# Performance work log

Hardware: AMD Instinct MI355X
Metric: run time of the kernel (lower is better)

Reference implementation:

```python
import jax, jax.numpy as jnp
import numpy as np
import math

B, S, D, H, WIDTH, NHW = 8, 1024, 512, 8, 8, 2
DK = D // H
S2 = S + 2 * WIDTH


def setup_inputs() -> dict:
    key = jax.random.key(0)
    ks = jax.random.split(key, 12)
    sc = 1.0 / math.sqrt(D)
    return {
        "x": jax.random.normal(ks[0], (B, S, D), jnp.float32),
        "l_attn_W": jax.random.normal(ks[1], (4, D, D), jnp.float32) * sc,  # q,k,v,out
        "l_attn_b": jnp.zeros((4, D), jnp.float32),
        "r_attn_W": jax.random.normal(ks[2], (4, D, D), jnp.float32) * sc,
        "r_attn_b": jnp.zeros((4, D), jnp.float32),
        "left_pad": jax.random.normal(ks[3], (WIDTH, D), jnp.float32) * sc,
        "right_pad": jax.random.normal(ks[4], (WIDTH, D), jnp.float32) * sc,
        "left_w": jax.random.normal(ks[5], (WIDTH + 1,), jnp.float32),
        "right_w": jax.random.normal(ks[6], (WIDTH + 1,), jnp.float32),
        "l_hw_W": jax.random.normal(ks[7], (NHW, D, 2 * D), jnp.float32) * sc,
        "l_hw_b": jnp.zeros((NHW, 2 * D), jnp.float32),
        "r_hw_W": jax.random.normal(ks[8], (NHW, D, 2 * D), jnp.float32) * sc,
        "r_hw_b": jnp.zeros((NHW, 2 * D), jnp.float32),
    }


def _mha(x, W, b, mask):
    # x: [B, S2, D]; W: [4, D, D]; mask: [1, S2, S2] bool (True = keep)
    q = (x @ W[0] + b[0]).reshape(B, S2, H, DK)
    k = (x @ W[1] + b[1]).reshape(B, S2, H, DK)
    v = (x @ W[2] + b[2]).reshape(B, S2, H, DK)
    scores = jnp.einsum('bihd,bjhd->bhij', q, k) / math.sqrt(DK)
    scores = jnp.where(mask[:, None], scores, jnp.float32(-1e9))
    p = jax.nn.softmax(scores, axis=-1)
    o = jnp.einsum('bhij,bjhd->bihd', p, v).reshape(B, S2, D)
    return o @ W[3] + b[3]


def _highway(x, Ws, bs):
    # AllenNLP-style Highway: projected -> [nonlinear | gate]
    for i in range(NHW):
        proj = x @ Ws[i] + bs[i]
        nl = jax.nn.relu(proj[..., :D])
        g = jax.nn.sigmoid(proj[..., D:])
        x = g * x + (1.0 - g) * nl
    return x


def reference(x, l_attn_W, l_attn_b, r_attn_W, r_attn_b, left_pad, right_pad,
              left_w, right_w, l_hw_W, l_hw_b, r_hw_W, r_hw_b):
    new_in = jnp.concatenate([
        jnp.broadcast_to(left_pad, (B, WIDTH, D)), x,
        jnp.broadcast_to(right_pad, (B, WIDTH, D))], axis=1)  # [B, S2, D]
    idx = jnp.arange(S2)
    diff = idx[:, None] - idx[None, :]
    lmask = ((diff >= 0) & (diff <= WIDTH + 1))[None]          # attend to [i-width-1, i]
    rmask = ((diff <= 0) & (diff >= -(WIDTH + 1)))[None]       # attend to [i, i+width+1]
    nl_attn = _mha(new_in, l_attn_W, l_attn_b, lmask)
    nr_attn = _mha(new_in, r_attn_W, r_attn_b, rmask)
    left_out = nl_attn[:, WIDTH:WIDTH + S, :]   # position end = start + width
    right_out = nr_attn[:, WIDTH:WIDTH + S, :]
    # relative-position weighted sliding windows (vectorized over all steps)
    lrel = sum(left_w[j] * new_in[:, j:j + S, :] for j in range(WIDTH + 1))
    rrel = sum(right_w[j] * new_in[:, WIDTH + j:WIDTH + j + S, :] for j in range(WIDTH + 1))
    left_out = _highway(left_out + lrel, l_hw_W, l_hw_b)
    right_out = _highway(right_out + rrel, r_hw_W, r_hw_b)
    out = jnp.concatenate([left_out, right_out], axis=-1)  # [B, S, 2D]
    return out[None]  # [1, B, S, 2D] matching torch stack layout
```

## Files before the change

### kernel.cpp

```cpp
#include <hip/hip_runtime.h>


#define B_ 8
#define S_ 1024
#define D_ 512
#define H_ 8
#define DK_ 64
#define WIDTH_ 8
#define S2_ 1040
#define NHW_ 2

typedef short bf16x8 __attribute__((ext_vector_type(8)));
typedef float f32x4 __attribute__((ext_vector_type(4)));

__device__ __forceinline__ float us2f(unsigned short u) {
  union { unsigned int i; float f; } c; c.i = ((unsigned int)u) << 16; return c.f;
}
__device__ __forceinline__ unsigned short f2us(float f) {
  union { float f; unsigned int i; } c; c.f = f;
  unsigned int x = c.i;
  return (unsigned short)((x + 0x7fffu + ((x >> 16) & 1u)) >> 16);
}
__device__ __forceinline__ unsigned int pack2(float a, float b) {
  return (unsigned int)f2us(a) | ((unsigned int)f2us(b) << 16);
}
__device__ __forceinline__ void async16(const void* g, void* l) {
  __builtin_amdgcn_global_load_lds(
      (const __attribute__((address_space(1))) void*)g,
      (__attribute__((address_space(3))) void*)l, 16, 0, 0);
}
__device__ __forceinline__ void unpack8(uint4 u, float* f) {
  unsigned int w[4] = {u.x, u.y, u.z, u.w};
  #pragma unroll
  for (int c = 0; c < 4; ++c) {
    union { unsigned int i; float g; } lo, hi;
    lo.i = w[c] << 16;
    hi.i = w[c] & 0xffff0000u;
    f[2 * c] = lo.g;
    f[2 * c + 1] = hi.g;
  }
}

__global__ __launch_bounds__(256) void k_prep(
    const float* __restrict__ x,
    const float* __restrict__ lpad, const float* __restrict__ rpad,
    const float* __restrict__ lW, const float* __restrict__ rW,
    const float* __restrict__ lb, const float* __restrict__ rb,
    const float* __restrict__ lhwW, const float* __restrict__ rhwW,
    unsigned short* __restrict__ WTall, unsigned short* __restrict__ WTp,
    unsigned short* __restrict__ hWT,
    unsigned short* __restrict__ nin, float* __restrict__ qkvbias)
{
  __shared__ float tile[32][33];
  const size_t DD = (size_t)D_ * D_;
  int bx = blockIdx.x;
  int tx = threadIdx.x & 31, ty = threadIdx.x >> 5;

  if (bx < 2048) {
    int sl = bx >> 8, rem = bx & 255;
    int side = sl >> 2, slice = sl & 3;
    int c0 = (rem & 15) * 32, r0 = (rem >> 4) * 32;
    const float* src = (side ? rW : lW) + (size_t)slice * DD;
    unsigned short* dst = (slice < 3) ? WTall + (size_t)(side * 3 + slice) * DD
                                      : WTp + (size_t)side * DD;
    #pragma unroll
    for (int i = 0; i < 4; ++i)
      tile[ty + i * 8][tx] = src[(size_t)(r0 + ty + i * 8) * D_ + c0 + tx];
    __syncthreads();
    #pragma unroll
    for (int i = 0; i < 4; ++i)
      dst[(size_t)(c0 + ty + i * 8) * D_ + r0 + tx] = f2us(tile[tx][ty + i * 8]);
    return;
  }
  if (bx < 4096) {
    int idx = bx - 2048;
    int sl = idx >> 9, rem = idx & 511;
    int c0 = (rem & 31) * 32, r0 = (rem >> 5) * 32;
    const float* src = ((sl >> 1) ? rhwW : lhwW) + (size_t)(sl & 1) * 512 * 1024;
    unsigned short* dst = hWT + (size_t)sl * 1024 * 512;
    #pragma unroll
    for (int i = 0; i < 4; ++i)
      tile[ty + i * 8][tx] = src[(size_t)(r0 + ty + i * 8) * 1024 + c0 + tx];
    __syncthreads();
    #pragma unroll
    for (int i = 0; i < 4; ++i) {
      int c = c0 + ty + i * 8;
      int q = (2 * ((c & 511) >> 4) + (c >= 512 ? 1 : 0)) * 16 + (c & 15);
      dst[(size_t)q * 512 + r0 + tx] = f2us(tile[tx][ty + i * 8]);
    }
    return;
  }
  int gid = (bx - 4096) * 256 + threadIdx.x;
  const int NTH = B_ * S2_ * 64;
  if (gid >= NTH) {
    int t = gid - NTH;
    if (t < 1536) qkvbias[t] = lb[t];
    else if (t < 3072) qkvbias[t] = rb[t - 1536];
    return;
  }
  int c8 = (gid & 63) << 3;
  int row = gid >> 6;
  int b = row / S2_;
  int t = row - b * S2_;
  const float* src;
  if (t < WIDTH_)            src = lpad + (size_t)t * D_ + c8;
  else if (t >= S_ + WIDTH_) src = rpad + (size_t)(t - S_ - WIDTH_) * D_ + c8;
  else                       src = x + ((size_t)b * S_ + (t - WIDTH_)) * D_ + c8;
  float4 a = *reinterpret_cast<const float4*>(src);
  float4 c = *reinterpret_cast<const float4*>(src + 4);
  uint4 o;
  o.x = pack2(a.x, a.y); o.y = pack2(a.z, a.w);
  o.z = pack2(c.x, c.y); o.w = pack2(c.z, c.w);
  *reinterpret_cast<uint4*>(nin + (size_t)row * D_ + c8) = o;
}

__global__ __launch_bounds__(256) void k_gemm_mfma(
    const unsigned short* __restrict__ A,
    const unsigned short* __restrict__ BT,
    const float* __restrict__ bias,
    unsigned short* __restrict__ C,
    int M, int N, int K)
{
  __shared__ unsigned short As[128 * 64];
  __shared__ unsigned short Bs[128 * 64];

  const int tid = threadIdx.x;
  const int w = tid >> 6;
  const int l = tid & 63;
  const int bm = blockIdx.y * 128;
  const int bn = blockIdx.x * 128;
  const int wrow = (w >> 1) * 64;
  const int wcol = (w & 1) * 64;

  const int lr = l >> 3;
  const int sk = (((l & 7) ^ lr) & 7) * 8;
  const unsigned short* Ap = A + (size_t)(bm + w * 8 + lr) * K + sk;
  const unsigned short* Bp = BT + (size_t)(bn + w * 8 + lr) * K + sk;
  unsigned short* lA = &As[w * 512];
  unsigned short* lB = &Bs[w * 512];
  const size_t K32 = (size_t)32 * K;

  const int fl = l & 15;
  const int fq = l >> 4;
  const int fx = fl & 7;

  f32x4 acc[4][4];
  #pragma unroll
  for (int mi = 0; mi < 4; ++mi)
    #pragma unroll
    for (int ni = 0; ni < 4; ++ni) acc[mi][ni] = (f32x4){0.f, 0.f, 0.f, 0.f};

  for (int k0 = 0; k0 < K; k0 += 64) {
    #pragma unroll
    for (int r = 0; r < 4; ++r) {
      async16(Ap + k0 + r * K32, lA + r * 2048);
      async16(Bp + k0 + r * K32, lB + r * 2048);
    }
    __syncthreads();
    #pragma unroll
    for (int s = 0; s < 2; ++s) {
      bf16x8 af[4], bfr[4];
      #pragma unroll
      for (int mi = 0; mi < 4; ++mi)
        af[mi] = *reinterpret_cast<const bf16x8*>(
            &As[(wrow + mi * 16 + fl) * 64 + (((s * 4 + fq) ^ fx) * 8)]);
      #pragma unroll
      for (int ni = 0; ni < 4; ++ni)
        bfr[ni] = *reinterpret_cast<const bf16x8*>(
            &Bs[(wcol + ni * 16 + fl) * 64 + (((s * 4 + fq) ^ fx) * 8)]);
      #pragma unroll
      for (int mi = 0; mi < 4; ++mi)
        #pragma unroll
        for (int ni = 0; ni < 4; ++ni)
          acc[mi][ni] = __builtin_amdgcn_mfma_f32_16x16x32_bf16(
              af[mi], bfr[ni], acc[mi][ni], 0, 0, 0);
    }
    __syncthreads();
  }

  float bv[4];
  #pragma unroll
  for (int ni = 0; ni < 4; ++ni) bv[ni] = bias[bn + wcol + ni * 16 + fl];

  const int rbase = (l >> 4) * 4;
  #pragma unroll
  for (int mi = 0; mi < 4; ++mi) {
    #pragma unroll
    for (int r = 0; r < 4; ++r) {
      int row = bm + wrow + mi * 16 + rbase + r;
      unsigned short* Cp = C + (size_t)row * N + bn + wcol + fl;
      #pragma unroll
      for (int ni = 0; ni < 4; ++ni)
        Cp[ni * 16] = f2us(acc[mi][ni][r] + bv[ni]);
    }
  }
}

__global__ __launch_bounds__(256) void k_gemm_proj(
    const unsigned short* __restrict__ ctx,
    const unsigned short* __restrict__ WTp,
    const unsigned short* __restrict__ nin,
    const float* __restrict__ lb3, const float* __restrict__ rb3,
    const float* __restrict__ wrel0, const float* __restrict__ wrel1,
    unsigned short* __restrict__ hwx)
{
  __shared__ unsigned short smem[128 * 136];
  unsigned short* As = smem;
  unsigned short* Bs = smem + 8192;
  const int K = 512, N = 512;
  const size_t MS = (size_t)B_ * S_ * D_;

  const int z = blockIdx.z;
  const unsigned short* A = ctx + (size_t)z * MS;
  const unsigned short* BT = WTp + (size_t)z * 512 * 512;
  const float* bias = z ? rb3 : lb3;
  const float* wrel = z ? wrel1 : wrel0;
  const int off = z * WIDTH_;

  const int tid = threadIdx.x;
  const int w = tid >> 6;
  const int l = tid & 63;
  const int bm = blockIdx.y * 128;
  const int bn = blockIdx.x * 128;
  const int wrow = (w >> 1) * 64;
  const int wcol = (w & 1) * 64;

  const int lr = l >> 3;
  const int sk = (((l & 7) ^ lr) & 7) * 8;
  const unsigned short* Ap = A + (size_t)(bm + w * 8 + lr) * K + sk;
  const unsigned short* Bp = BT + (size_t)(bn + w * 8 + lr) * K + sk;
  unsigned short* lA = &As[w * 512];
  unsigned short* lB = &Bs[w * 512];
  const size_t K32 = (size_t)32 * K;

  const int fl = l & 15;
  const int fq = l >> 4;
  const int fx = fl & 7;

  f32x4 acc[4][4];
  #pragma unroll
  for (int mi = 0; mi < 4; ++mi)
    #pragma unroll
    for (int ni = 0; ni < 4; ++ni) acc[mi][ni] = (f32x4){0.f, 0.f, 0.f, 0.f};

  for (int k0 = 0; k0 < K; k0 += 64) {
    #pragma unroll
    for (int r = 0; r < 4; ++r) {
      async16(Ap + k0 + r * K32, lA + r * 2048);
      async16(Bp + k0 + r * K32, lB + r * 2048);
    }
    __syncthreads();
    #pragma unroll
    for (int s = 0; s < 2; ++s) {
      bf16x8 af[4], bfr[4];
      #pragma unroll
      for (int mi = 0; mi < 4; ++mi)
        af[mi] = *reinterpret_cast<const bf16x8*>(
            &As[(wrow + mi * 16 + fl) * 64 + (((s * 4 + fq) ^ fx) * 8)]);
      #pragma unroll
      for (int ni = 0; ni < 4; ++ni)
        bfr[ni] = *reinterpret_cast<const bf16x8*>(
            &Bs[(wcol + ni * 16 + fl) * 64 + (((s * 4 + fq) ^ fx) * 8)]);
      #pragma unroll
      for (int mi = 0; mi < 4; ++mi)
        #pragma unroll
        for (int ni = 0; ni < 4; ++ni)
          acc[mi][ni] = __builtin_amdgcn_mfma_f32_16x16x32_bf16(
              af[mi], bfr[ni], acc[mi][ni], 0, 0, 0);
    }
    __syncthreads();
  }

  float bv[4];
  #pragma unroll
  for (int ni = 0; ni < 4; ++ni) bv[ni] = bias[bn + wcol + ni * 16 + fl];
  const int rbase = (l >> 4) * 4;
  #pragma unroll
  for (int mi = 0; mi < 4; ++mi)
    #pragma unroll
    for (int r = 0; r < 4; ++r)
      #pragma unroll
      for (int ni = 0; ni < 4; ++ni)
        smem[(wrow + mi * 16 + rbase + r) * 136 + wcol + ni * 16 + fl] =
            f2us(acc[mi][ni][r] + bv[ni]);
  __syncthreads();

  const int trow = tid >> 4;
  const int tcol = (tid & 15) * 8;
  const float w0 = wrel[0], w1 = wrel[1], w2 = wrel[2], w3 = wrel[3],
              w4 = wrel[4], w5 = wrel[5], w6 = wrel[6], w7 = wrel[7],
              w8 = wrel[8];
  const float wj[9] = {w0, w1, w2, w3, w4, w5, w6, w7, w8};
  #pragma unroll
  for (int i = 0; i < 8; ++i) {
    int r = trow + i * 16;
    int gr = bm + r;
    int b = gr >> 10, s = gr & (S_ - 1);
    float a8[8];
    unpack8(*reinterpret_cast<const uint4*>(&smem[r * 136 + tcol]), a8);
    const unsigned short* np =
        nin + ((size_t)b * S2_ + off + s) * D_ + bn + tcol;
    #pragma unroll
    for (int j = 0; j < 9; ++j) {
      float nf[8];
      unpack8(*reinterpret_cast<const uint4*>(np + (size_t)j * D_), nf);
      #pragma unroll
      for (int e = 0; e < 8; ++e) a8[e] += wj[j] * nf[e];
    }
    uint4 o;
    o.x = pack2(a8[0], a8[1]); o.y = pack2(a8[2], a8[3]);
    o.z = pack2(a8[4], a8[5]); o.w = pack2(a8[6], a8[7]);
    *reinterpret_cast<uint4*>(
        hwx + (size_t)z * MS + (size_t)gr * D_ + bn + tcol) = o;
  }
}

template <bool FINAL>
__global__ __launch_bounds__(256) void k_gemm_hw(
    const unsigned short* __restrict__ Xsrc,
    const unsigned short* __restrict__ BT, size_t bStrZ,
    const float* __restrict__ bias0, const float* __restrict__ bias1,
    unsigned short* __restrict__ Obf,
    float* __restrict__ Ofp)
{
  __shared__ unsigned short As[128 * 64];
  __shared__ unsigned short Bs[128 * 64];
  const int K = 512;
  const size_t MS = (size_t)B_ * S_ * D_;

  const int z = blockIdx.z;
  const unsigned short* A = Xsrc + (size_t)z * MS;
  BT += (size_t)z * bStrZ;
  const float* bias = z ? bias1 : bias0;

  const int tid = threadIdx.x;
  const int w = tid >> 6;
  const int l = tid & 63;
  const int bm = blockIdx.y * 128;
  const int bn = blockIdx.x * 128;
  const int wrow = (w >> 1) * 64;
  const int wcol = (w & 1) * 64;

  const int lr = l >> 3;
  const int sk = (((l & 7) ^ lr) & 7) * 8;
  const unsigned short* Ap = A + (size_t)(bm + w * 8 + lr) * K + sk;
  const unsigned short* Bp = BT + (size_t)(bn + w * 8 + lr) * K + sk;
  unsigned short* lA = &As[w * 512];
  unsigned short* lB = &Bs[w * 512];
  const size_t K32 = (size_t)32 * K;

  const int fl = l & 15;
  const int fq = l >> 4;
  const int fx = fl & 7;

  f32x4 acc[4][4];
  #pragma unroll
  for (int mi = 0; mi < 4; ++mi)
    #pragma unroll
    for (int ni = 0; ni < 4; ++ni) acc[mi][ni] = (f32x4){0.f, 0.f, 0.f, 0.f};

  for (int k0 = 0; k0 < K; k0 += 64) {
    #pragma unroll
    for (int r = 0; r < 4; ++r) {
      async16(Ap + k0 + r * K32, lA + r * 2048);
      async16(Bp + k0 + r * K32, lB + r * 2048);
    }
    __syncthreads();
    #pragma unroll
    for (int s = 0; s < 2; ++s) {
      bf16x8 af[4], bfr[4];
      #pragma unroll
      for (int mi = 0; mi < 4; ++mi)
        af[mi] = *reinterpret_cast<const bf16x8*>(
            &As[(wrow + mi * 16 + fl) * 64 + (((s * 4 + fq) ^ fx) * 8)]);
      #pragma unroll
      for (int ni = 0; ni < 4; ++ni)
        bfr[ni] = *reinterpret_cast<const bf16x8*>(
            &Bs[(wcol + ni * 16 + fl) * 64 + (((s * 4 + fq) ^ fx) * 8)]);
      #pragma unroll
      for (int mi = 0; mi < 4; ++mi)
        #pragma unroll
        for (int ni = 0; ni < 4; ++ni)
          acc[mi][ni] = __builtin_amdgcn_mfma_f32_16x16x32_bf16(
              af[mi], bfr[ni], acc[mi][ni], 0, 0, 0);
    }
    __syncthreads();
  }

  const int ocb = ((bn + wcol) >> 1) + fl;
  float bnl[2], bg[2];
  #pragma unroll
  for (int p = 0; p < 2; ++p) {
    bnl[p] = bias[ocb + p * 16];
    bg[p]  = bias[512 + ocb + p * 16];
  }

  const int rbase = (l >> 4) * 4;
  #pragma unroll
  for (int mi = 0; mi < 4; ++mi) {
    #pragma unroll
    for (int r = 0; r < 4; ++r) {
      int row = bm + wrow + mi * 16 + rbase + r;
      #pragma unroll
      for (int p = 0; p < 2; ++p) {
        int oc = ocb + p * 16;
        float nl = fmaxf(acc[mi][2 * p][r] + bnl[p], 0.f);
        float g  = 1.f / (1.f + __expf(-(acc[mi][2 * p + 1][r] + bg[p])));
        float xv = us2f(A[(size_t)row * 512 + oc]);
        float res = g * xv + (1.f - g) * nl;
        if (FINAL) Ofp[(size_t)row * 1024 + z * 512 + oc] = res;
        else       Obf[(size_t)z * MS + (size_t)row * 512 + oc] = f2us(res);
      }
    }
  }
}

__global__ __launch_bounds__(256) void k_attn_window(
    const unsigned short* __restrict__ qkv,
    unsigned short* __restrict__ ctx)
{
  int wid = (blockIdx.x * 256 + threadIdx.x) >> 6;
  int lane = threadIdx.x & 63;
  int s = wid & (S_ - 1);
  int b = (wid >> 10) & (B_ - 1);
  int dir = wid >> 13;
  int i = s + WIDTH_;

  const size_t base = (size_t)b * S2_ * 3072 + dir * 1536;
  const int c0 = lane * 8;

  float qf[8];
  unpack8(*reinterpret_cast<const uint4*>(qkv + base + (size_t)i * 3072 + c0), qf);

  float sc[10];
  float mx = -1e30f;
  #pragma unroll
  for (int t = 0; t < 10; ++t) {
    int j = (dir == 0) ? (i - 9 + t) : (i + t);
    float sv = -1e30f;
    if (j >= 0 && j < S2_) {
      float kf[8];
      unpack8(*reinterpret_cast<const uint4*>(
          qkv + base + (size_t)j * 3072 + 512 + c0), kf);
      float p = qf[0] * kf[0];
      #pragma unroll
      for (int e = 1; e < 8; ++e) p += qf[e] * kf[e];
      p += __shfl_xor(p, 1);
      p += __shfl_xor(p, 2);
      p += __shfl_xor(p, 4);
      sv = p * 0.125f;
    }
    sc[t] = sv;
    mx = fmaxf(mx, sv);
  }

  float denom = 0.f;
  #pragma unroll
  for (int t = 0; t < 10; ++t) {
    sc[t] = (sc[t] > -1e29f) ? __expf(sc[t] - mx) : 0.f;
    denom += sc[t];
  }
  float inv = 1.f / denom;

  float acc[8] = {0.f, 0.f, 0.f, 0.f, 0.f, 0.f, 0.f, 0.f};
  #pragma unroll
  for (int t = 0; t < 10; ++t) {
    int j = (dir == 0) ? (i - 9 + t) : (i + t);
    if (j >= 0 && j < S2_) {
      float vf[8];
      unpack8(*reinterpret_cast<const uint4*>(
          qkv + base + (size_t)j * 3072 + 1024 + c0), vf);
      float p = sc[t];
      #pragma unroll
      for (int e = 0; e < 8; ++e) acc[e] += p * vf[e];
    }
  }

  uint4 o;
  o.x = pack2(acc[0] * inv, acc[1] * inv);
  o.y = pack2(acc[2] * inv, acc[3] * inv);
  o.z = pack2(acc[4] * inv, acc[5] * inv);
  o.w = pack2(acc[6] * inv, acc[7] * inv);
  *reinterpret_cast<uint4*>(
      ctx + (((size_t)dir * B_ + b) * S_ + s) * D_ + c0) = o;
}

extern "C" void kernel_launch(void* const* d_in, const int* in_sizes, int n_in,
                              void* d_out, int out_size, void* d_ws, size_t ws_size,
                              hipStream_t stream) {
  const float* x    = (const float*)d_in[0];
  const float* lW   = (const float*)d_in[1];
  const float* lb   = (const float*)d_in[2];
  const float* rW   = (const float*)d_in[3];
  const float* rb   = (const float*)d_in[4];
  const float* lpad = (const float*)d_in[5];
  const float* rpad = (const float*)d_in[6];
  const float* lw   = (const float*)d_in[7];
  const float* rw   = (const float*)d_in[8];
  const float* lhwW = (const float*)d_in[9];
  const float* lhwb = (const float*)d_in[10];
  const float* rhwW = (const float*)d_in[11];
  const float* rhwb = (const float*)d_in[12];
  float* out = (float*)d_out;
  unsigned short* ws = (unsigned short*)d_ws;

  const size_t NIN  = (size_t)B_ * S2_ * D_;
  const size_t NQKV = (size_t)B_ * S2_ * 3072;
  const size_t MS   = (size_t)B_ * S_ * D_;
  const size_t DD   = (size_t)D_ * D_;
  const size_t LHW  = (size_t)1024 * 512;

  unsigned short* nin   = ws;
  unsigned short* qkv   = nin + NIN;
  unsigned short* ctx   = qkv + NQKV;
  unsigned short* hwx   = ctx + 2 * MS;
  unsigned short* hwy   = hwx + 2 * MS;
  unsigned short* WTall = hwy + 2 * MS;
  unsigned short* WTp   = WTall + 6 * DD;
  unsigned short* hWT   = WTp + 2 * DD;
  float* qkvbias        = (float*)(hWT + 4 * LHW);

  k_prep<<<6188, 256, 0, stream>>>(x, lpad, rpad, lW, rW, lb, rb, lhwW, rhwW,
                                   WTall, WTp, hWT, nin, qkvbias);

  const int MQ = B_ * S2_;

  {
    dim3 g(3072 / 128, MQ / 128, 1);
    k_gemm_mfma<<<g, 256, 0, stream>>>(nin, WTall, qkvbias, qkv, MQ, 3072, D_);
  }

  k_attn_window<<<(2 * B_ * S_) / 4, 256, 0, stream>>>(qkv, ctx);

  {
    dim3 g(D_ / 128, (B_ * S_) / 128, 2);
    k_gemm_proj<<<g, 256, 0, stream>>>(ctx, WTp, nin, lb + 3 * D_, rb + 3 * D_,
                                       lw, rw, hwx);
  }

  {
    dim3 g(1024 / 128, (B_ * S_) / 128, 2);
    k_gemm_hw<false><<<g, 256, 0, stream>>>(hwx, hWT, 2 * LHW,
                                            lhwb, rhwb, hwy, nullptr);
    k_gemm_hw<true><<<g, 256, 0, stream>>>(hwy, hWT + LHW, 2 * LHW,
                                           lhwb + 1024, rhwb + 1024,
                                           nullptr, out);
  }
}
```

Before: 249.1 us.

## Reuse K/V and window rows across queries, remap GEMM tiles per XCD, split prep

The windowed attention kernel now has each wave handle four consecutive query rows. K/V rows loaded once are shared across overlapping windows instead of being reloaded per query. The projection epilogue likewise computes the relative-position sum for four rows from a shared set of 12 loaded neighbour rows. The QKV and highway GEMMs remap block indices so consecutive tiles land on the same XCD for better L2 locality. The highway kernel stages its residual input tile in LDS via async loads instead of scattered global reads, and the prep kernel is split into weight and activation kernels, adding one extra launch.

```diff
diff --git a/kernel.cpp b/kernel.cpp
--- a/kernel.cpp
+++ b/kernel.cpp
@@ -41,15 +41,11 @@
   }
 }
 
-__global__ __launch_bounds__(256) void k_prep(
-    const float* __restrict__ x,
-    const float* __restrict__ lpad, const float* __restrict__ rpad,
+__global__ __launch_bounds__(256) void k_prep_w(
     const float* __restrict__ lW, const float* __restrict__ rW,
-    const float* __restrict__ lb, const float* __restrict__ rb,
     const float* __restrict__ lhwW, const float* __restrict__ rhwW,
     unsigned short* __restrict__ WTall, unsigned short* __restrict__ WTp,
-    unsigned short* __restrict__ hWT,
-    unsigned short* __restrict__ nin, float* __restrict__ qkvbias)
+    unsigned short* __restrict__ hWT)
 {
   __shared__ float tile[32][33];
   const size_t DD = (size_t)D_ * D_;
@@ -72,25 +68,30 @@
       dst[(size_t)(c0 + ty + i * 8) * D_ + r0 + tx] = f2us(tile[tx][ty + i * 8]);
     return;
   }
-  if (bx < 4096) {
-    int idx = bx - 2048;
-    int sl = idx >> 9, rem = idx & 511;
-    int c0 = (rem & 31) * 32, r0 = (rem >> 5) * 32;
-    const float* src = ((sl >> 1) ? rhwW : lhwW) + (size_t)(sl & 1) * 512 * 1024;
-    unsigned short* dst = hWT + (size_t)sl * 1024 * 512;
-    #pragma unroll
-    for (int i = 0; i < 4; ++i)
-      tile[ty + i * 8][tx] = src[(size_t)(r0 + ty + i * 8) * 1024 + c0 + tx];
-    __syncthreads();
-    #pragma unroll
-    for (int i = 0; i < 4; ++i) {
-      int c = c0 + ty + i * 8;
-      int q = (2 * ((c & 511) >> 4) + (c >= 512 ? 1 : 0)) * 16 + (c & 15);
-      dst[(size_t)q * 512 + r0 + tx] = f2us(tile[tx][ty + i * 8]);
-    }
-    return;
-  }
-  int gid = (bx - 4096) * 256 + threadIdx.x;
+  int idx = bx - 2048;
+  int sl = idx >> 9, rem = idx & 511;
+  int c0 = (rem & 31) * 32, r0 = (rem >> 5) * 32;
+  const float* src = ((sl >> 1) ? rhwW : lhwW) + (size_t)(sl & 1) * 512 * 1024;
+  unsigned short* dst = hWT + (size_t)sl * 1024 * 512;
+  #pragma unroll
+  for (int i = 0; i < 4; ++i)
+    tile[ty + i * 8][tx] = src[(size_t)(r0 + ty + i * 8) * 1024 + c0 + tx];
+  __syncthreads();
+  #pragma unroll
+  for (int i = 0; i < 4; ++i) {
+    int c = c0 + ty + i * 8;
+    int q = (2 * ((c & 511) >> 4) + (c >= 512 ? 1 : 0)) * 16 + (c & 15);
+    dst[(size_t)q * 512 + r0 + tx] = f2us(tile[tx][ty + i * 8]);
+  }
+}
+
+__global__ __launch_bounds__(256) void k_prep_x(
+    const float* __restrict__ x,
+    const float* __restrict__ lpad, const float* __restrict__ rpad,
+    const float* __restrict__ lb, const float* __restrict__ rb,
+    unsigned short* __restrict__ nin, float* __restrict__ qkvbias)
+{
+  int gid = blockIdx.x * 256 + threadIdx.x;
   const int NTH = B_ * S2_ * 64;
   if (gid >= NTH) {
     int t = gid - NTH;
@@ -127,8 +128,15 @@
   const int tid = threadIdx.x;
   const int w = tid >> 6;
   const int l = tid & 63;
-  const int bm = blockIdx.y * 128;
-  const int bn = blockIdx.x * 128;
+
+  const int gx = gridDim.x;
+  const int nwg = gx * gridDim.y;
+  const int flat = blockIdx.y * gx + blockIdx.x;
+  const int cpx = nwg >> 3;
+  const int nf = (flat & 7) * cpx + (flat >> 3);
+  const int bm = (nf / gx) * 128;
+  const int bn = (nf % gx) * 128;
+
   const int wrow = (w >> 1) * 64;
   const int wcol = (w & 1) * 64;
 
@@ -192,6 +200,127 @@
       #pragma unroll
       for (int ni = 0; ni < 4; ++ni)
         Cp[ni * 16] = f2us(acc[mi][ni][r] + bv[ni]);
+    }
+  }
+}
+
+template <bool FINAL>
+__global__ __launch_bounds__(256) void k_gemm_hw(
+    const unsigned short* __restrict__ Xsrc,
+    const unsigned short* __restrict__ BTb, size_t bStrZ,
+    const float* __restrict__ bias0, const float* __restrict__ bias1,
+    unsigned short* __restrict__ Obf,
+    float* __restrict__ Ofp)
+{
+  __shared__ unsigned short As[128 * 64];
+  __shared__ unsigned short Bs[128 * 64];
+  const int K = 512;
+  const size_t MS = (size_t)B_ * S_ * D_;
+
+  const int z = blockIdx.z;
+  const unsigned short* A = Xsrc + (size_t)z * MS;
+  const unsigned short* BT = BTb + (size_t)z * bStrZ;
+  const float* bias = z ? bias1 : bias0;
+
+  const int tid = threadIdx.x;
+  const int w = tid >> 6;
+  const int l = tid & 63;
+
+  const int gx = gridDim.x;
+  const int nwg = gx * gridDim.y;
+  const int flat = blockIdx.y * gx + blockIdx.x;
+  const int cpx = nwg >> 3;
+  const int nf = (flat & 7) * cpx + (flat >> 3);
+  const int bm = (nf / gx) * 128;
+  const int bn = (nf % gx) * 128;
+
+  const int wrow = (w >> 1) * 64;
+  const int wcol = (w & 1) * 64;
+
+  const int lr = l >> 3;
+  const int sk = (((l & 7) ^ lr) & 7) * 8;
+  const unsigned short* Ap = A + (size_t)(bm + w * 8 + lr) * K + sk;
+  const unsigned short* Bp = BT + (size_t)(bn + w * 8 + lr) * K + sk;
+  unsigned short* lA = &As[w * 512];
+  unsigned short* lB = &Bs[w * 512];
+  const size_t K32 = (size_t)32 * K;
+
+  const int fl = l & 15;
+  const int fq = l >> 4;
+  const int fx = fl & 7;
+
+  f32x4 acc[4][4];
+  #pragma unroll
+  for (int mi = 0; mi < 4; ++mi)
+    #pragma unroll
+    for (int ni = 0; ni < 4; ++ni) acc[mi][ni] = (f32x4){0.f, 0.f, 0.f, 0.f};
+
+  for (int k0 = 0; k0 < K; k0 += 64) {
+    #pragma unroll
+    for (int r = 0; r < 4; ++r) {
+      async16(Ap + k0 + r * K32, lA + r * 2048);
+      async16(Bp + k0 + r * K32, lB + r * 2048);
+    }
+    __syncthreads();
+    #pragma unroll
+    for (int s = 0; s < 2; ++s) {
+      bf16x8 af[4], bfr[4];
+      #pragma unroll
+      for (int mi = 0; mi < 4; ++mi)
+        af[mi] = *reinterpret_cast<const bf16x8*>(
+            &As[(wrow + mi * 16 + fl) * 64 + (((s * 4 + fq) ^ fx) * 8)]);
+      #pragma unroll
+      for (int ni = 0; ni < 4; ++ni)
+        bfr[ni] = *reinterpret_cast<const bf16x8*>(
+            &Bs[(wcol + ni * 16 + fl) * 64 + (((s * 4 + fq) ^ fx) * 8)]);
+      #pragma unroll
+      for (int mi = 0; mi < 4; ++mi)
+        #pragma unroll
+        for (int ni = 0; ni < 4; ++ni)
+          acc[mi][ni] = __builtin_amdgcn_mfma_f32_16x16x32_bf16(
+              af[mi], bfr[ni], acc[mi][ni], 0, 0, 0);
+    }
+    __syncthreads();
+  }
+
+  {
+    const unsigned short* gs = A + (size_t)bm * 512 + (bn >> 1);
+    #pragma unroll
+    for (int i = 0; i < 4; ++i) {
+      int row = i * 32 + (tid >> 3);
+      int cb = tid & 7;
+      int ss = (cb * 8) ^ ((row & 12) << 2);
+      async16(gs + (size_t)row * 512 + ss, &As[row * 64 + cb * 8]);
+    }
+  }
+  asm volatile("s_waitcnt vmcnt(0)" ::: "memory");
+  __syncthreads();
+
+  const int ocb = ((bn + wcol) >> 1) + fl;
+  float bnl[2], bg[2];
+  #pragma unroll
+  for (int p = 0; p < 2; ++p) {
+    bnl[p] = bias[ocb + p * 16];
+    bg[p]  = bias[512 + ocb + p * 16];
+  }
+  const int rbase = fq * 4;
+  const int crel0 = (wcol >> 1) + fl;
+  #pragma unroll
+  for (int mi = 0; mi < 4; ++mi) {
+    #pragma unroll
+    for (int r = 0; r < 4; ++r) {
+      int lrow = wrow + mi * 16 + rbase + r;
+      int row = bm + lrow;
+      #pragma unroll
+      for (int p = 0; p < 2; ++p) {
+        int oc = ocb + p * 16;
+        float xv = us2f(As[lrow * 64 + ((crel0 + p * 16) ^ ((lrow & 12) << 2))]);
+        float nl = fmaxf(acc[mi][2 * p][r] + bnl[p], 0.f);
+        float g  = 1.f / (1.f + __expf(-(acc[mi][2 * p + 1][r] + bg[p])));
+        float res = g * xv + (1.f - g) * nl;
+        if (FINAL) Ofp[(size_t)row * 1024 + z * 512 + oc] = res;
+        else       Obf[(size_t)z * MS + (size_t)row * 512 + oc] = f2us(res);
+      }
     }
   }
 }
@@ -207,7 +336,7 @@
   __shared__ unsigned short smem[128 * 136];
   unsigned short* As = smem;
   unsigned short* Bs = smem + 8192;
-  const int K = 512, N = 512;
+  const int K = 512;
   const size_t MS = (size_t)B_ * S_ * D_;
 
   const int z = blockIdx.z;
@@ -285,131 +414,42 @@
             f2us(acc[mi][ni][r] + bv[ni]);
   __syncthreads();
 
-  const int trow = tid >> 4;
+  const float wj[9] = {wrel[0], wrel[1], wrel[2], wrel[3], wrel[4],
+                       wrel[5], wrel[6], wrel[7], wrel[8]};
+  const int g8 = (tid >> 4) * 8;
   const int tcol = (tid & 15) * 8;
-  const float w0 = wrel[0], w1 = wrel[1], w2 = wrel[2], w3 = wrel[3],
-              w4 = wrel[4], w5 = wrel[5], w6 = wrel[6], w7 = wrel[7],
-              w8 = wrel[8];
-  const float wj[9] = {w0, w1, w2, w3, w4, w5, w6, w7, w8};
-  #pragma unroll
-  for (int i = 0; i < 8; ++i) {
-    int r = trow + i * 16;
-    int gr = bm + r;
-    int b = gr >> 10, s = gr & (S_ - 1);
-    float a8[8];
-    unpack8(*reinterpret_cast<const uint4*>(&smem[r * 136 + tcol]), a8);
+  {
+    int gr0 = bm + g8;
+    int b0 = gr0 >> 10, s0 = gr0 & (S_ - 1);
     const unsigned short* np =
-        nin + ((size_t)b * S2_ + off + s) * D_ + bn + tcol;
-    #pragma unroll
-    for (int j = 0; j < 9; ++j) {
-      float nf[8];
-      unpack8(*reinterpret_cast<const uint4*>(np + (size_t)j * D_), nf);
-      #pragma unroll
-      for (int e = 0; e < 8; ++e) a8[e] += wj[j] * nf[e];
-    }
-    uint4 o;
-    o.x = pack2(a8[0], a8[1]); o.y = pack2(a8[2], a8[3]);
-    o.z = pack2(a8[4], a8[5]); o.w = pack2(a8[6], a8[7]);
-    *reinterpret_cast<uint4*>(
-        hwx + (size_t)z * MS + (size_t)gr * D_ + bn + tcol) = o;
-  }
-}
-
-template <bool FINAL>
-__global__ __launch_bounds__(256) void k_gemm_hw(
-    const unsigned short* __restrict__ Xsrc,
-    const unsigned short* __restrict__ BT, size_t bStrZ,
-    const float* __restrict__ bias0, const float* __restrict__ bias1,
-    unsigned short* __restrict__ Obf,
-    float* __restrict__ Ofp)
-{
-  __shared__ unsigned short As[128 * 64];
-  __shared__ unsigned short Bs[128 * 64];
-  const int K = 512;
-  const size_t MS = (size_t)B_ * S_ * D_;
-
-  const int z = blockIdx.z;
-  const unsigned short* A = Xsrc + (size_t)z * MS;
-  BT += (size_t)z * bStrZ;
-  const float* bias = z ? bias1 : bias0;
-
-  const int tid = threadIdx.x;
-  const int w = tid >> 6;
-  const int l = tid & 63;
-  const int bm = blockIdx.y * 128;
-  const int bn = blockIdx.x * 128;
-  const int wrow = (w >> 1) * 64;
-  const int wcol = (w & 1) * 64;
-
-  const int lr = l >> 3;
-  const int sk = (((l & 7) ^ lr) & 7) * 8;
-  const unsigned short* Ap = A + (size_t)(bm + w * 8 + lr) * K + sk;
-  const unsigned short* Bp = BT + (size_t)(bn + w * 8 + lr) * K + sk;
-  unsigned short* lA = &As[w * 512];
-  unsigned short* lB = &Bs[w * 512];
-  const size_t K32 = (size_t)32 * K;
-
-  const int fl = l & 15;
-  const int fq = l >> 4;
-  const int fx = fl & 7;
-
-  f32x4 acc[4][4];
-  #pragma unroll
-  for (int mi = 0; mi < 4; ++mi)
-    #pragma unroll
-    for (int ni = 0; ni < 4; ++ni) acc[mi][ni] = (f32x4){0.f, 0.f, 0.f, 0.f};
-
-  for (int k0 = 0; k0 < K; k0 += 64) {
-    #pragma unroll
-    for (int r = 0; r < 4; ++r) {
-      async16(Ap + k0 + r * K32, lA + r * 2048);
-      async16(Bp + k0 + r * K32, lB + r * 2048);
-    }
-    __syncthreads();
-    #pragma unroll
-    for (int s = 0; s < 2; ++s) {
-      bf16x8 af[4], bfr[4];
-      #pragma unroll
-      for (int mi = 0; mi < 4; ++mi)
-        af[mi] = *reinterpret_cast<const bf16x8*>(
-            &As[(wrow + mi * 16 + fl) * 64 + (((s * 4 + fq) ^ fx) * 8)]);
-      #pragma unroll
-      for (int ni = 0; ni < 4; ++ni)
-        bfr[ni] = *reinterpret_cast<const bf16x8*>(
-            &Bs[(wcol + ni * 16 + fl) * 64 + (((s * 4 + fq) ^ fx) * 8)]);
-      #pragma unroll
-      for (int mi = 0; mi < 4; ++mi)
+        nin + ((size_t)b0 * S2_ + off + s0) * D_ + bn + tcol;
+    unsigned short* op = hwx + (size_t)z * MS + (size_t)gr0 * D_ + bn + tcol;
+    #pragma unroll
+    for (int h = 0; h < 2; ++h) {
+      float a4[4][8];
+      #pragma unroll
+      for (int i = 0; i < 4; ++i)
+        unpack8(*reinterpret_cast<const uint4*>(
+            &smem[(g8 + h * 4 + i) * 136 + tcol]), a4[i]);
+      #pragma unroll
+      for (int t = 0; t < 12; ++t) {
+        float nf[8];
+        unpack8(*reinterpret_cast<const uint4*>(
+            np + (size_t)(h * 4 + t) * D_), nf);
         #pragma unroll
-        for (int ni = 0; ni < 4; ++ni)
-          acc[mi][ni] = __builtin_amdgcn_mfma_f32_16x16x32_bf16(
-              af[mi], bfr[ni], acc[mi][ni], 0, 0, 0);
-    }
-    __syncthreads();
-  }
-
-  const int ocb = ((bn + wcol) >> 1) + fl;
-  float bnl[2], bg[2];
-  #pragma unroll
-  for (int p = 0; p < 2; ++p) {
-    bnl[p] = bias[ocb + p * 16];
-    bg[p]  = bias[512 + ocb + p * 16];
-  }
-
-  const int rbase = (l >> 4) * 4;
-  #pragma unroll
-  for (int mi = 0; mi < 4; ++mi) {
-    #pragma unroll
-    for (int r = 0; r < 4; ++r) {
-      int row = bm + wrow + mi * 16 + rbase + r;
-      #pragma unroll
-      for (int p = 0; p < 2; ++p) {
-        int oc = ocb + p * 16;
-        float nl = fmaxf(acc[mi][2 * p][r] + bnl[p], 0.f);
-        float g  = 1.f / (1.f + __expf(-(acc[mi][2 * p + 1][r] + bg[p])));
-        float xv = us2f(A[(size_t)row * 512 + oc]);
-        float res = g * xv + (1.f - g) * nl;
-        if (FINAL) Ofp[(size_t)row * 1024 + z * 512 + oc] = res;
-        else       Obf[(size_t)z * MS + (size_t)row * 512 + oc] = f2us(res);
+        for (int i = 0; i < 4; ++i) {
+          if (t < i || t > i + 8) continue;
+          float wv = wj[t - i];
+          #pragma unroll
+          for (int e = 0; e < 8; ++e) a4[i][e] += wv * nf[e];
+        }
+      }
+      #pragma unroll
+      for (int i = 0; i < 4; ++i) {
+        uint4 o;
+        o.x = pack2(a4[i][0], a4[i][1]); o.y = pack2(a4[i][2], a4[i][3]);
+        o.z = pack2(a4[i][4], a4[i][5]); o.w = pack2(a4[i][6], a4[i][7]);
+        *reinterpret_cast<uint4*>(op + (size_t)(h * 4 + i) * D_) = o;
       }
     }
   }
@@ -421,68 +461,96 @@
 {
   int wid = (blockIdx.x * 256 + threadIdx.x) >> 6;
   int lane = threadIdx.x & 63;
-  int s = wid & (S_ - 1);
-  int b = (wid >> 10) & (B_ - 1);
-  int dir = wid >> 13;
-  int i = s + WIDTH_;
+  int sg = wid & 255;
+  int b = (wid >> 8) & 7;
+  int dir = wid >> 11;
+  int s0 = sg << 2;
+  int i0 = s0 + WIDTH_;
 
   const size_t base = (size_t)b * S2_ * 3072 + dir * 1536;
   const int c0 = lane * 8;
 
-  float qf[8];
-  unpack8(*reinterpret_cast<const uint4*>(qkv + base + (size_t)i * 3072 + c0), qf);
-
-  float sc[10];
-  float mx = -1e30f;
-  #pragma unroll
-  for (int t = 0; t < 10; ++t) {
-    int j = (dir == 0) ? (i - 9 + t) : (i + t);
-    float sv = -1e30f;
-    if (j >= 0 && j < S2_) {
-      float kf[8];
+  float qf[4][8];
+  #pragma unroll
+  for (int r = 0; r < 4; ++r)
+    unpack8(*reinterpret_cast<const uint4*>(
+        qkv + base + (size_t)(i0 + r) * 3072 + c0), qf[r]);
+
+  float sc[4][10];
+  float mx[4] = {-1e30f, -1e30f, -1e30f, -1e30f};
+  #pragma unroll
+  for (int t = 0; t < 13; ++t) {
+    int j = (dir == 0) ? (i0 - 9 + t) : (i0 + t);
+    bool ok = (j >= 0 && j < S2_);
+    float kf[8];
+    if (ok)
       unpack8(*reinterpret_cast<const uint4*>(
           qkv + base + (size_t)j * 3072 + 512 + c0), kf);
-      float p = qf[0] * kf[0];
-      #pragma unroll
-      for (int e = 1; e < 8; ++e) p += qf[e] * kf[e];
-      p += __shfl_xor(p, 1);
-      p += __shfl_xor(p, 2);
-      p += __shfl_xor(p, 4);
-      sv = p * 0.125f;
-    }
-    sc[t] = sv;
-    mx = fmaxf(mx, sv);
-  }
-
-  float denom = 0.f;
-  #pragma unroll
-  for (int t = 0; t < 10; ++t) {
-    sc[t] = (sc[t] > -1e29f) ? __expf(sc[t] - mx) : 0.f;
-    denom += sc[t];
-  }
-  float inv = 1.f / denom;
-
-  float acc[8] = {0.f, 0.f, 0.f, 0.f, 0.f, 0.f, 0.f, 0.f};
-  #pragma unroll
-  for (int t = 0; t < 10; ++t) {
-    int j = (dir == 0) ? (i - 9 + t) : (i + t);
-    if (j >= 0 && j < S2_) {
-      float vf[8];
+    #pragma unroll
+    for (int r = 0; r < 4; ++r) {
+      if (t < r || t > r + 9) continue;
+      float sv = -1e30f;
+      if (ok) {
+        float p = qf[r][0] * kf[0];
+        #pragma unroll
+        for (int e = 1; e < 8; ++e) p += qf[r][e] * kf[e];
+        p += __shfl_xor(p, 1);
+        p += __shfl_xor(p, 2);
+        p += __shfl_xor(p, 4);
+        sv = p * 0.125f;
+      }
+      sc[r][t - r] = sv;
+      mx[r] = fmaxf(mx[r], sv);
+    }
+  }
+
+  float inv[4];
+  #pragma unroll
+  for (int r = 0; r < 4; ++r) {
+    float den = 0.f;
+    #pragma unroll
+    for (int u = 0; u < 10; ++u) {
+      sc[r][u] = (sc[r][u] > -1e29f) ? __expf(sc[r][u] - mx[r]) : 0.f;
+      den += sc[r][u];
+    }
+    inv[r] = 1.f / den;
+  }
+
+  float acc[4][8];
+  #pragma unroll
+  for (int r = 0; r < 4; ++r)
+    #pragma unroll
+    for (int e = 0; e < 8; ++e) acc[r][e] = 0.f;
+
+  #pragma unroll
+  for (int t = 0; t < 13; ++t) {
+    int j = (dir == 0) ? (i0 - 9 + t) : (i0 + t);
+    bool ok = (j >= 0 && j < S2_);
+    float vf[8];
+    if (ok)
       unpack8(*reinterpret_cast<const uint4*>(
           qkv + base + (size_t)j * 3072 + 1024 + c0), vf);
-      float p = sc[t];
-      #pragma unroll
-      for (int e = 0; e < 8; ++e) acc[e] += p * vf[e];
-    }
-  }
-
-  uint4 o;
-  o.x = pack2(acc[0] * inv, acc[1] * inv);
-  o.y = pack2(acc[2] * inv, acc[3] * inv);
-  o.z = pack2(acc[4] * inv, acc[5] * inv);
-  o.w = pack2(acc[6] * inv, acc[7] * inv);
-  *reinterpret_cast<uint4*>(
-      ctx + (((size_t)dir * B_ + b) * S_ + s) * D_ + c0) = o;
+    #pragma unroll
+    for (int r = 0; r < 4; ++r) {
+      if (t < r || t > r + 9) continue;
+      if (ok) {
+        float p = sc[r][t - r];
+        #pragma unroll
+        for (int e = 0; e < 8; ++e) acc[r][e] += p * vf[e];
+      }
+    }
+  }
+
+  #pragma unroll
+  for (int r = 0; r < 4; ++r) {
+    uint4 o;
+    o.x = pack2(acc[r][0] * inv[r], acc[r][1] * inv[r]);
+    o.y = pack2(acc[r][2] * inv[r], acc[r][3] * inv[r]);
+    o.z = pack2(acc[r][4] * inv[r], acc[r][5] * inv[r]);
+    o.w = pack2(acc[r][6] * inv[r], acc[r][7] * inv[r]);
+    *reinterpret_cast<uint4*>(
+        ctx + (((size_t)dir * B_ + b) * S_ + s0 + r) * D_ + c0) = o;
+  }
 }
 
 extern "C" void kernel_launch(void* const* d_in, const int* in_sizes, int n_in,
@@ -520,8 +588,8 @@
   unsigned short* hWT   = WTp + 2 * DD;
   float* qkvbias        = (float*)(hWT + 4 * LHW);
 
-  k_prep<<<6188, 256, 0, stream>>>(x, lpad, rpad, lW, rW, lb, rb, lhwW, rhwW,
-                                   WTall, WTp, hWT, nin, qkvbias);
+  k_prep_w<<<4096, 256, 0, stream>>>(lW, rW, lhwW, rhwW, WTall, WTp, hWT);
+  k_prep_x<<<2092, 256, 0, stream>>>(x, lpad, rpad, lb, rb, nin, qkvbias);
 
   const int MQ = B_ * S2_;
 
@@ -530,7 +598,7 @@
     k_gemm_mfma<<<g, 256, 0, stream>>>(nin, WTall, qkvbias, qkv, MQ, 3072, D_);
   }
 
-  k_attn_window<<<(2 * B_ * S_) / 4, 256, 0, stream>>>(qkv, ctx);
+  k_attn_window<<<(2 * B_ * S_) / 16, 256, 0, stream>>>(qkv, ctx);
 
   {
     dim3 g(D_ / 128, (B_ * S_) / 128, 2);
```

Result: faster. 234.5 us (-5.9%).
